# Kernel tuning notes

Measured on AMD Instinct MI355X. Metric: run time of the kernel, lower is better.

## Reference

```python
import jax, jax.numpy as jnp
import numpy as np

HEADS = 12
ROT_DIM = 16  # hidden_dim // num_heads // 4
MAX_FREQ = 256
EPS = 1e-5


def _groupnorm(x, w, b, groups, eps=EPS):
    # x: [B, C, H, W, D]; normalize per (group, H, W, D)
    B, C = x.shape[0], x.shape[1]
    xr = x.reshape(B, groups, -1)
    mu = xr.mean(-1, keepdims=True)
    var = xr.var(-1, keepdims=True)
    xn = ((xr - mu) * jax.lax.rsqrt(var + eps)).reshape(x.shape)
    return xn * w.reshape(1, C, 1, 1, 1) + b.reshape(1, C, 1, 1, 1)


def _layernorm(t, w, b, eps=EPS):
    mu = t.mean(-1, keepdims=True)
    var = t.var(-1, keepdims=True)
    return (t - mu) * jax.lax.rsqrt(var + eps) * w + b


def _rotate_half(t):
    # pairs adjacent elements: (x1, x2) -> (-x2, x1)
    x1 = t[..., 0::2]
    x2 = t[..., 1::2]
    return jnp.stack([-x2, x1], axis=-1).reshape(t.shape)


def _axial_freqs(H, W, D, dim=ROT_DIM, max_freq=MAX_FREQ):
    # 'pixel' rotary: base freqs = linspace(1, max_freq/2, dim//2) * pi, pos in [-1, 1]
    base = jnp.linspace(1.0, max_freq / 2.0, dim // 2) * jnp.pi

    def ax(n):
        pos = jnp.linspace(-1.0, 1.0, n)
        f = pos[:, None] * base[None, :]          # [n, dim//2]
        return jnp.repeat(f, 2, axis=-1)           # [n, dim]

    fh = jnp.broadcast_to(ax(H)[:, None, None, :], (H, W, D, dim))
    fw = jnp.broadcast_to(ax(W)[None, :, None, :], (H, W, D, dim))
    fd = jnp.broadcast_to(ax(D)[None, None, :, :], (H, W, D, dim))
    return jnp.concatenate([fh, fw, fd], -1)       # [H, W, D, 3*dim]


def _rope(freqs, t):
    # t: [B, he, H, W, D, hd]; rotate first rot dims, pass rest through
    rot = freqs.shape[-1]
    tl, tr = t[..., :rot], t[..., rot:]
    tl = tl * jnp.cos(freqs) + _rotate_half(tl) * jnp.sin(freqs)
    return jnp.concatenate([tl, tr], -1)


def setup_inputs() -> dict:
    key = jax.random.key(0)
    ks = jax.random.split(key, 14)
    B, C, H, W, D = 2, 768, 16, 16, 8
    hd = C // HEADS
    f32 = jnp.float32
    inp = {
        "x": jax.random.normal(ks[0], (B, C, H, W, D), f32),
        "norm1_w": 1.0 + 0.1 * jax.random.normal(ks[1], (C,), f32),
        "norm1_b": 0.1 * jax.random.normal(ks[2], (C,), f32),
        "gamma_att": 0.01 * jnp.ones((C,), f32),
        "W_fused": jax.random.normal(ks[3], (C, 7 * C), f32) / np.sqrt(C),
        "b_fused": 0.01 * jax.random.normal(ks[4], (7 * C,), f32),
        "qn_w": 1.0 + 0.1 * jax.random.normal(ks[5], (hd,), f32),
        "qn_b": 0.1 * jax.random.normal(ks[6], (hd,), f32),
        "kn_w": 1.0 + 0.1 * jax.random.normal(ks[7], (hd,), f32),
        "kn_b": 0.1 * jax.random.normal(ks[8], (hd,), f32),
        "W_attn": jax.random.normal(ks[9], (C, C), f32) / np.sqrt(C),
        "W_ffout": jax.random.normal(ks[10], (2 * C, C), f32) / np.sqrt(2 * C),
        "b_ffout": 0.01 * jax.random.normal(ks[11], (C,), f32),
        "bcs": 0,
        "axis_order": 0,
    }
    return inp


def reference(x, norm1_w, norm1_b, gamma_att, W_fused, b_fused, qn_w, qn_b,
              kn_w, kn_b, W_attn, W_ffout, b_ffout, bcs, axis_order):
    B, C, H, W, D = x.shape
    he = HEADS
    hd = C // he
    x_in = x

    # GroupNorm over channels (num_groups = num_heads)
    xn = _groupnorm(x, norm1_w, norm1_b, he)
    t = jnp.transpose(xn, (0, 2, 3, 4, 1))             # b h w d c

    fused = t @ W_fused + b_fused                      # b h w d 7C
    ff, q, k, v = jnp.split(fused, [4 * C, 5 * C, 6 * C], axis=-1)

    def to_heads(z):
        return z.reshape(B, H, W, D, he, hd).transpose(0, 4, 1, 2, 3, 5)  # b he h w d c

    q, k, v = to_heads(q), to_heads(k), to_heads(v)
    q = _layernorm(q, qn_w, qn_b)
    k = _layernorm(k, kn_w, kn_b)

    freqs = _axial_freqs(H, W, D)                      # [H, W, D, 48]
    q = _rope(freqs, q)
    k = _rope(freqs, k)

    S = H * W * D
    qf = q.reshape(B, he, S, hd)
    kf = k.reshape(B, he, S, hd)
    vf = v.reshape(B, he, S, hd)

    scale = 1.0 / np.sqrt(hd)
    scores = jnp.einsum('bhqc,bhkc->bhqk', qf, kf) * scale
    attn = jax.nn.softmax(scores, axis=-1)
    out = jnp.einsum('bhqk,bhkc->bhqc', attn, vf)      # b he S hd

    att = out.reshape(B, he, H, W, D, hd).transpose(0, 2, 3, 4, 1, 5).reshape(B, H, W, D, C)
    att_out = att @ W_attn

    # SwiGLU: first half is value, second half gates
    xh, gate = jnp.split(ff, 2, axis=-1)
    ff_out = (jax.nn.silu(gate) * xh) @ W_ffout + b_ffout

    y = gamma_att * (att_out + ff_out)                 # b h w d c
    return jnp.transpose(y, (0, 4, 1, 2, 3)) + x_in    # b c h w d
```

## Files before the change

kernel.cpp:

```cpp
#include <hip/hip_runtime.h>
#include <hip/hip_bf16.h>

#define HE   12
#define HD   64
#define Cc   768
#define C2   1536
#define C4   3072
#define N7   5376
#define Bb   2
#define Ss   2048
#define BSr  4096
#define PI_F 3.14159265358979f

using f32x4  = __attribute__((ext_vector_type(4))) float;
using short8 = __attribute__((ext_vector_type(8))) short;

__device__ __forceinline__ unsigned short f2b(float f) {
    union { float f; unsigned int u; } v; v.f = f;
    unsigned int u = v.u;
    unsigned int r = (u + 0x7fffu + ((u >> 16) & 1u)) >> 16;
    return (unsigned short)r;
}
__device__ __forceinline__ unsigned short f2bt(float f) {
    union { float f; unsigned int u; } v; v.f = f;
    return (unsigned short)(v.u >> 16);
}
__device__ __forceinline__ float b2f(unsigned short s) {
    union { unsigned int u; float f; } v; v.u = ((unsigned int)s) << 16;
    return v.f;
}
__device__ __forceinline__ f32x4 mfma16(short8 a, short8 b, f32x4 c) {
    return __builtin_amdgcn_mfma_f32_16x16x32_bf16(a, b, c, 0, 0, 0);
}
__device__ __forceinline__ void gl_lds16(const unsigned short* g, unsigned short* l) {
    __builtin_amdgcn_global_load_lds(
        (const __attribute__((address_space(1))) unsigned int*)(const void*)g,
        (__attribute__((address_space(3))) unsigned int*)(void*)l, 16, 0, 0);
}
__device__ __forceinline__ void xcd_tile(int& bx, int& by) {
    int nx = gridDim.x;
    int flat = blockIdx.y * nx + blockIdx.x;
    int nwg = nx * gridDim.y;
    int swz = (flat & 7) * (nwg >> 3) + (flat >> 3);
    bx = swz % nx; by = swz / nx;
}

union U8 { uint4 v; unsigned short u[8]; };

__global__ __launch_bounds__(256) void transpose_w(const float* __restrict__ src,
                                                   unsigned short* __restrict__ dst,
                                                   int R, int Ccol) {
    __shared__ float tile[32][33];
    int tx = threadIdx.x & 31, ty = threadIdx.x >> 5;
    int rt = blockIdx.y * 32, ct = blockIdx.x * 32;
#pragma unroll
    for (int i = 0; i < 4; ++i)
        tile[ty + i * 8][tx] = src[(size_t)(rt + ty + i * 8) * Ccol + ct + tx];
    __syncthreads();
#pragma unroll
    for (int i = 0; i < 4; ++i)
        dst[(size_t)(ct + ty + i * 8) * R + rt + tx] = f2b(tile[tx][ty + i * 8]);
}

__global__ __launch_bounds__(256) void gn_stats(const float* __restrict__ x,
                                                float* __restrict__ stat) {
    int j = blockIdx.x;
    const float4* p = (const float4*)(x + (size_t)j * 131072);
    float s = 0.f, ss = 0.f;
    for (int i = threadIdx.x; i < 32768; i += 256) {
        float4 v = p[i];
        s  += v.x + v.y + v.z + v.w;
        ss += v.x * v.x + v.y * v.y + v.z * v.z + v.w * v.w;
    }
#pragma unroll
    for (int m = 1; m < 64; m <<= 1) { s += __shfl_xor(s, m); ss += __shfl_xor(ss, m); }
    __shared__ float ls[4], lss[4];
    int wid = threadIdx.x >> 6;
    if ((threadIdx.x & 63) == 0) { ls[wid] = s; lss[wid] = ss; }
    __syncthreads();
    if (threadIdx.x == 0) {
        s = ls[0] + ls[1] + ls[2] + ls[3];
        ss = lss[0] + lss[1] + lss[2] + lss[3];
        float mu  = s / 131072.0f;
        float var = ss / 131072.0f - mu * mu;
        stat[j * 2]     = mu;
        stat[j * 2 + 1] = rsqrtf(var + 1e-5f);
    }
}

__global__ __launch_bounds__(256) void norm_transpose(const float* __restrict__ x,
                                                      const float* __restrict__ stat,
                                                      const float* __restrict__ w,
                                                      const float* __restrict__ bgn,
                                                      unsigned short* __restrict__ t) {
    __shared__ float tile[32][33];
    int b = blockIdx.z;
    int st = blockIdx.x * 32, ct = blockIdx.y * 32;
    int tx = threadIdx.x & 31, ty = threadIdx.x >> 5;
#pragma unroll
    for (int i = 0; i < 4; ++i) {
        int c = ct + ty + i * 8;
        int g = c >> 6;
        float mu = stat[(b * 12 + g) * 2], rs = stat[(b * 12 + g) * 2 + 1];
        float v = x[(size_t)(b * Cc + c) * Ss + st + tx];
        tile[ty + i * 8][tx] = (v - mu) * rs * w[c] + bgn[c];
    }
    __syncthreads();
#pragma unroll
    for (int i = 0; i < 4; ++i) {
        int s = st + ty + i * 8, c = ct + tx;
        t[(size_t)(b * Ss + s) * Cc + c] = f2b(tile[tx][ty + i * 8]);
    }
}

template<bool ACCUM, bool BIAS, bool OUTBF16>
__global__ __launch_bounds__(256) void gemm128(const unsigned short* __restrict__ A,
                                               const unsigned short* __restrict__ Bt,
                                               const float* __restrict__ bias,
                                               void* __restrict__ Cout,
                                               int M, int N, int K) {
    __shared__ __align__(16) unsigned short As[128 * 32];
    __shared__ __align__(16) unsigned short Bs[128 * 32];
    const int tid = threadIdx.x;
    const int wid = tid >> 6, lane = tid & 63;
    const int lr = lane & 15, lh = lane >> 4;
    const int wr = wid >> 1, wc = wid & 1;
    int bx, by; xcd_tile(bx, by);
    const int row0 = by * 128, col0 = bx * 128;
    const unsigned short* ga = A  + (size_t)(row0 + (tid >> 2)) * K + (tid & 3) * 8;
    const unsigned short* gb = Bt + (size_t)(col0 + (tid >> 2)) * K + (tid & 3) * 8;
    f32x4 acc[4][4] = {};

    for (int k0 = 0; k0 < K; k0 += 32) {
        gl_lds16(ga + k0,          &As[tid * 8]);
        gl_lds16(ga + 64 * K + k0, &As[2048 + tid * 8]);
        gl_lds16(gb + k0,          &Bs[tid * 8]);
        gl_lds16(gb + 64 * K + k0, &Bs[2048 + tid * 8]);
        __syncthreads();
        short8 af[4], bfr[4];
#pragma unroll
        for (int m = 0; m < 4; ++m) af[m]  = *(const short8*)&As[(wr * 64 + m * 16 + lr) * 32 + lh * 8];
#pragma unroll
        for (int n = 0; n < 4; ++n) bfr[n] = *(const short8*)&Bs[(wc * 64 + n * 16 + lr) * 32 + lh * 8];
#pragma unroll
        for (int m = 0; m < 4; ++m)
#pragma unroll
            for (int n = 0; n < 4; ++n)
                acc[m][n] = mfma16(af[m], bfr[n], acc[m][n]);
        __syncthreads();
    }

#pragma unroll
    for (int m = 0; m < 4; ++m)
#pragma unroll
        for (int n = 0; n < 4; ++n) {
            int row = row0 + wr * 64 + m * 16 + lh * 4;
            int col = col0 + wc * 64 + n * 16 + lr;
            float bv = BIAS ? bias[col] : 0.0f;
#pragma unroll
            for (int r = 0; r < 4; ++r) {
                size_t idx = (size_t)(row + r) * N + col;
                float v = acc[m][n][r] + bv;
                if (ACCUM) v += ((const float*)Cout)[idx];
                if (OUTBF16) ((unsigned short*)Cout)[idx] = f2b(v);
                else         ((float*)Cout)[idx] = v;
            }
        }
}

__global__ __launch_bounds__(256) void gemm_fin(const unsigned short* __restrict__ A,
                                                const unsigned short* __restrict__ Bt,
                                                const float* __restrict__ bo,
                                                const float* __restrict__ oaccIn,
                                                const float* __restrict__ x,
                                                const float* __restrict__ gamma,
                                                float* __restrict__ out,
                                                int M, int N, int K) {
    __shared__ __align__(16) unsigned short As[128 * 32];
    __shared__ __align__(16) unsigned short Bs[128 * 32];
    const int tid = threadIdx.x;
    const int wid = tid >> 6, lane = tid & 63;
    const int lr = lane & 15, lh = lane >> 4;
    const int wr = wid >> 1, wc = wid & 1;
    int bx, by; xcd_tile(bx, by);
    const int row0 = by * 128, col0 = bx * 128;
    const unsigned short* ga = A  + (size_t)(row0 + (tid >> 2)) * K + (tid & 3) * 8;
    const unsigned short* gb = Bt + (size_t)(col0 + (tid >> 2)) * K + (tid & 3) * 8;
    f32x4 acc[4][4] = {};

    for (int k0 = 0; k0 < K; k0 += 32) {
        gl_lds16(ga + k0,          &As[tid * 8]);
        gl_lds16(ga + 64 * K + k0, &As[2048 + tid * 8]);
        gl_lds16(gb + k0,          &Bs[tid * 8]);
        gl_lds16(gb + 64 * K + k0, &Bs[2048 + tid * 8]);
        __syncthreads();
        short8 af[4], bfr[4];
#pragma unroll
        for (int m = 0; m < 4; ++m) af[m]  = *(const short8*)&As[(wr * 64 + m * 16 + lr) * 32 + lh * 8];
#pragma unroll
        for (int n = 0; n < 4; ++n) bfr[n] = *(const short8*)&Bs[(wc * 64 + n * 16 + lr) * 32 + lh * 8];
#pragma unroll
        for (int m = 0; m < 4; ++m)
#pragma unroll
            for (int n = 0; n < 4; ++n)
                acc[m][n] = mfma16(af[m], bfr[n], acc[m][n]);
        __syncthreads();
    }

#pragma unroll
    for (int m = 0; m < 4; ++m)
#pragma unroll
        for (int n = 0; n < 4; ++n) {
            int row = row0 + wr * 64 + m * 16 + lh * 4;
            int col = col0 + wc * 64 + n * 16 + lr;
            float bv = bo[col], gv = gamma[col];
#pragma unroll
            for (int r = 0; r < 4; ++r) {
                int rw = row + r;
                float v = acc[m][n][r] + bv + oaccIn[(size_t)rw * N + col];
                int b = rw >> 11, s = rw & 2047;
                size_t oidx = (size_t)(b * Cc + col) * Ss + s;
                out[oidx] = gv * v + x[oidx];
            }
        }
}

__global__ __launch_bounds__(256) void qkv_prep(const unsigned short* __restrict__ fused,
                                                const float* __restrict__ qnw, const float* __restrict__ qnb,
                                                const float* __restrict__ knw, const float* __restrict__ knb,
                                                unsigned short* __restrict__ qf,
                                                unsigned short* __restrict__ kf,
                                                unsigned short* __restrict__ vf) {
    const int wid = threadIdx.x >> 6, lane = threadIdx.x & 63;
    const int job = blockIdx.x * 4 + wid;
    const int srow = job / 12, h = job % 12;
    const int b = srow >> 11, s = srow & 2047;

    size_t base = (size_t)srow * N7 + C4 + h * HD;
    float qv = b2f(fused[base + lane]);
    float kv = b2f(fused[base + Cc + lane]);
    float vv = b2f(fused[base + 2 * Cc + lane]);

    float qs = qv, ks = kv;
#pragma unroll
    for (int m = 1; m < 64; m <<= 1) { qs += __shfl_xor(qs, m); ks += __shfl_xor(ks, m); }
    float qmu = qs * (1.0f / 64.0f), kmu = ks * (1.0f / 64.0f);
    float qd = qv - qmu, kd = kv - kmu;
    float qv2 = qd * qd, kv2 = kd * kd;
#pragma unroll
    for (int m = 1; m < 64; m <<= 1) { qv2 += __shfl_xor(qv2, m); kv2 += __shfl_xor(kv2, m); }
    float qn = qd * rsqrtf(qv2 * (1.0f / 64.0f) + 1e-5f) * qnw[lane] + qnb[lane];
    float kn = kd * rsqrtf(kv2 * (1.0f / 64.0f) + 1e-5f) * knw[lane] + knb[lane];

    if (lane < 48) {
        int axis = lane >> 4, ii = (lane & 15) >> 1;
        float basef = (1.0f + (float)ii * (127.0f / 7.0f)) * PI_F;
        int   pos_i = (axis == 0) ? (s >> 7) : (axis == 1) ? ((s >> 3) & 15) : (s & 7);
        float denom = (axis == 2) ? 7.0f : 15.0f;
        float pos   = -1.0f + 2.0f * (float)pos_i / denom;
        float ang   = pos * basef;
        float sn, cs;
        sincosf(ang, &sn, &cs);
        float qp = __shfl_xor(qn, 1);
        float kp = __shfl_xor(kn, 1);
        qn = (lane & 1) ? (qn * cs + qp * sn) : (qn * cs - qp * sn);
        kn = (lane & 1) ? (kn * cs + kp * sn) : (kn * cs - kp * sn);
    }

    size_t obase = ((size_t)(b * 12 + h) * Ss + s) * HD + lane;
    qf[obase] = f2b(qn);
    kf[obase] = f2b(kn);
    vf[obase] = f2b(vv);
}

__global__ __launch_bounds__(256) void ffa_prep(const unsigned short* __restrict__ fused,
                                                unsigned short* __restrict__ ffa) {
    int i8 = blockIdx.x * 256 + threadIdx.x;
    int row = i8 / 192, co = (i8 % 192) * 8;
    U8 xa, ga, oa;
    xa.v = *(const uint4*)&fused[(size_t)row * N7 + co];
    ga.v = *(const uint4*)&fused[(size_t)row * N7 + C2 + co];
#pragma unroll
    for (int j = 0; j < 8; ++j) {
        float g = b2f(ga.u[j]);
        float xh = b2f(xa.u[j]);
        float sg = 1.0f / (1.0f + __expf(-g));
        oa.u[j] = f2b(g * sg * xh);
    }
    *(uint4*)&ffa[(size_t)row * C2 + co] = oa.v;
}

__global__ __launch_bounds__(256) void attn64(const unsigned short* __restrict__ qf,
                                              const unsigned short* __restrict__ kf,
                                              const unsigned short* __restrict__ vf,
                                              unsigned short* __restrict__ att) {
    __shared__ __align__(16) unsigned short Ks[2][64][80];
    __shared__ __align__(16) unsigned short Vt[2][64][80];
    __shared__ __align__(16) unsigned short Ps[4][16][80];
    const int tid = threadIdx.x, wid = tid >> 6, lane = tid & 63;
    const int lr = lane & 15, lh = lane >> 4;
    const int bh = blockIdx.y, qt = blockIdx.x;
    const int b = bh / 12, h = bh % 12;
    const size_t kvbase = (size_t)bh * Ss * HD;

    const int qrow = qt * 64 + wid * 16 + lr;
    short8 qa0 = *(const short8*)&qf[kvbase + (size_t)qrow * HD + lh * 8];
    short8 qa1 = *(const short8*)&qf[kvbase + (size_t)qrow * HD + 32 + lh * 8];

    const int r0 = tid >> 3, kc0 = (tid & 7) * 8;
    const int sv0 = (((r0 >> 3) ^ (kc0 >> 3)) << 3) | (r0 & 7);
    const int sv1 = ((((r0 >> 3) + 4) ^ (kc0 >> 3)) << 3) | (r0 & 7);
    const unsigned short* kptr = kf + kvbase + (size_t)r0 * HD + kc0;
    const unsigned short* vptr = vf + kvbase + (size_t)r0 * HD + kc0;

    const short8 ones = {0x3F80, 0x3F80, 0x3F80, 0x3F80, 0x3F80, 0x3F80, 0x3F80, 0x3F80};
    const float c1 = 0.125f * 1.44269504f;
    const float c2 = 23.08312065f;
    const int rxb = (lr >> 2) & 3;

    f32x4 oacc[4] = {};
    f32x4 lacc = {};

    uint4 kreg0 = *(const uint4*)kptr;
    uint4 kreg1 = *(const uint4*)(kptr + 32 * HD);
    U8 vreg0, vreg1;
    vreg0.v = *(const uint4*)vptr;
    vreg1.v = *(const uint4*)(vptr + 32 * HD);
    *(uint4*)&Ks[0][r0][kc0]      = kreg0;
    *(uint4*)&Ks[0][r0 + 32][kc0] = kreg1;
#pragma unroll
    for (int j = 0; j < 8; ++j) Vt[0][kc0 + j][sv0] = vreg0.u[j];
#pragma unroll
    for (int j = 0; j < 8; ++j) Vt[0][kc0 + j][sv1] = vreg1.u[j];
    kreg0   = *(const uint4*)(kptr + 64 * HD);
    kreg1   = *(const uint4*)(kptr + 96 * HD);
    vreg0.v = *(const uint4*)(vptr + 64 * HD);
    vreg1.v = *(const uint4*)(vptr + 96 * HD);
    __syncthreads();

#pragma unroll 2
    for (int kt = 0; kt < 32; ++kt) {
        const int cur = kt & 1;
        if (kt < 31) {
            *(uint4*)&Ks[cur ^ 1][r0][kc0]      = kreg0;
            *(uint4*)&Ks[cur ^ 1][r0 + 32][kc0] = kreg1;
#pragma unroll
            for (int j = 0; j < 8; ++j) Vt[cur ^ 1][kc0 + j][sv0] = vreg0.u[j];
#pragma unroll
            for (int j = 0; j < 8; ++j) Vt[cur ^ 1][kc0 + j][sv1] = vreg1.u[j];
        }
        if (kt < 30) {
            const unsigned short* kp = kptr + (size_t)(kt + 2) * 64 * HD;
            const unsigned short* vp = vptr + (size_t)(kt + 2) * 64 * HD;
            kreg0   = *(const uint4*)kp;
            kreg1   = *(const uint4*)(kp + 32 * HD);
            vreg0.v = *(const uint4*)vp;
            vreg1.v = *(const uint4*)(vp + 32 * HD);
        }

        f32x4 sc[4];
#pragma unroll
        for (int n = 0; n < 4; ++n) {
            f32x4 z = {0.f, 0.f, 0.f, 0.f};
            short8 k0 = *(const short8*)&Ks[cur][n * 16 + lr][lh * 8];
            short8 k1 = *(const short8*)&Ks[cur][n * 16 + lr][32 + lh * 8];
            z = mfma16(qa0, k0, z);
            z = mfma16(qa1, k1, z);
            sc[n] = z;
        }

#pragma unroll
        for (int n = 0; n < 4; ++n)
#pragma unroll
            for (int r = 0; r < 4; ++r)
                sc[n][r] = exp2f(sc[n][r] * c1 - c2);

#pragma unroll
        for (int r = 0; r < 4; ++r) {
            int prow = lh * 4 + r;
            int lo = lr & 7, lr3 = lr >> 3;
            Ps[wid][prow][(((0 + lr3) ^ lh) << 3) | lo] = f2bt(sc[0][r]);
            Ps[wid][prow][(((2 + lr3) ^ lh) << 3) | lo] = f2bt(sc[1][r]);
            Ps[wid][prow][(((4 + lr3) ^ lh) << 3) | lo] = f2bt(sc[2][r]);
            Ps[wid][prow][(((6 + lr3) ^ lh) << 3) | lo] = f2bt(sc[3][r]);
        }

        short8 pa0 = *(const short8*)&Ps[wid][lr][((lh ^ rxb) & 7) * 8];
        short8 pa1 = *(const short8*)&Ps[wid][lr][(((lh + 4) ^ rxb) & 7) * 8];
        lacc = mfma16(pa0, ones, lacc);
        lacc = mfma16(pa1, ones, lacc);
#pragma unroll
        for (int n = 0; n < 4; ++n) {
            int dv = (2 * n + (lr >> 3)) & 7;
            short8 v0 = *(const short8*)&Vt[cur][n * 16 + lr][((lh ^ dv) & 7) * 8];
            short8 v1 = *(const short8*)&Vt[cur][n * 16 + lr][(((lh + 4) ^ dv) & 7) * 8];
            oacc[n] = mfma16(pa0, v0, oacc[n]);
            oacc[n] = mfma16(pa1, v1, oacc[n]);
        }
        __syncthreads();
    }

    float rinv[4];
#pragma unroll
    for (int r = 0; r < 4; ++r) rinv[r] = 1.0f / lacc[r];
#pragma unroll
    for (int n = 0; n < 4; ++n)
#pragma unroll
        for (int r = 0; r < 4; ++r) {
            int srow_w = qt * 64 + wid * 16 + lh * 4 + r;
            int col = h * HD + n * 16 + lr;
            att[(size_t)(b * Ss + srow_w) * Cc + col] = f2b(oacc[n][r] * rinv[r]);
        }
}

extern "C" void kernel_launch(void* const* d_in, const int* in_sizes, int n_in,
                              void* d_out, int out_size, void* d_ws, size_t ws_size,
                              hipStream_t stream) {
    const float* x     = (const float*)d_in[0];
    const float* n1w   = (const float*)d_in[1];
    const float* n1b   = (const float*)d_in[2];
    const float* gamma = (const float*)d_in[3];
    const float* Wf    = (const float*)d_in[4];
    const float* bfu   = (const float*)d_in[5];
    const float* qnw   = (const float*)d_in[6];
    const float* qnb   = (const float*)d_in[7];
    const float* knw   = (const float*)d_in[8];
    const float* knb   = (const float*)d_in[9];
    const float* Wa    = (const float*)d_in[10];
    const float* Wo    = (const float*)d_in[11];
    const float* bo    = (const float*)d_in[12];

    char* ws = (char*)d_ws;
    size_t off = 0;
    auto alloc = [&](size_t bytes) {
        char* p = ws + off;
        off = (off + bytes + 255) & ~(size_t)255;
        return p;
    };
    float*          stat  = (float*)alloc(24 * 2 * 4);
    unsigned short* t     = (unsigned short*)alloc((size_t)BSr * Cc * 2);
    unsigned short* WtF   = (unsigned short*)alloc((size_t)N7 * Cc * 2);
    unsigned short* fused = (unsigned short*)alloc((size_t)BSr * N7 * 2);
    unsigned short* qfB   = (unsigned short*)alloc((size_t)Bb * HE * Ss * HD * 2);
    unsigned short* kfB   = (unsigned short*)alloc((size_t)Bb * HE * Ss * HD * 2);
    unsigned short* vfB   = (unsigned short*)alloc((size_t)Bb * HE * Ss * HD * 2);
    unsigned short* ffa   = (unsigned short*)alloc((size_t)BSr * C2 * 2);
    unsigned short* WtA   = (unsigned short*)alloc((size_t)Cc * Cc * 2);
    unsigned short* WtO   = (unsigned short*)alloc((size_t)Cc * C2 * 2);
    unsigned short* attB  = t;
    float*          oacc  = (float*)fused;

    transpose_w<<<dim3(N7 / 32, Cc / 32), 256, 0, stream>>>(Wf, WtF, Cc, N7);
    transpose_w<<<dim3(Cc / 32, Cc / 32), 256, 0, stream>>>(Wa, WtA, Cc, Cc);
    transpose_w<<<dim3(Cc / 32, C2 / 32), 256, 0, stream>>>(Wo, WtO, C2, Cc);

    gn_stats<<<24, 256, 0, stream>>>(x, stat);
    norm_transpose<<<dim3(Ss / 32, Cc / 32, Bb), 256, 0, stream>>>(x, stat, n1w, n1b, t);

    gemm128<false, true, true><<<dim3(N7 / 128, BSr / 128), 256, 0, stream>>>(
        t, WtF, bfu, fused, BSr, N7, Cc);

    qkv_prep<<<(Bb * Ss * HE) / 4, 256, 0, stream>>>(fused, qnw, qnb, knw, knb, qfB, kfB, vfB);
    ffa_prep<<<(BSr * C2 / 8) / 256, 256, 0, stream>>>(fused, ffa);

    attn64<<<dim3(Ss / 64, Bb * HE), 256, 0, stream>>>(qfB, kfB, vfB, attB);

    gemm128<false, false, false><<<dim3(Cc / 128, BSr / 128), 256, 0, stream>>>(
        attB, WtA, nullptr, oacc, BSr, Cc, Cc);
    gemm_fin<<<dim3(Cc / 128, BSr / 128), 256, 0, stream>>>(
        ffa, WtO, bo, oacc, x, gamma, (float*)d_out, BSr, Cc, C2);
}
```

Measured before the change: 370.8 us.

## Split attention over key halves with combine kernel; double-buffer and swizzle GEMM LDS

Attention is split into two key-range halves via a third grid dimension, each writing unnormalized fp32 partial outputs and row sums to scratch, followed by a combine kernel that sums, normalizes and converts to bf16. This doubles block count to better fill the GPU, at the cost of extra scratch traffic and removal of the attention kernel's LDS double buffering. The GEMM kernels get double-buffered LDS staging with one barrier per step and an XOR swizzle of k-chunks to reduce bank conflicts. Correctness relies on the softmax using a fixed scale without running max, so partials can be summed directly.

```diff
diff --git a/kernel.cpp b/kernel.cpp
--- a/kernel.cpp
+++ b/kernel.cpp
@@ -119,29 +119,40 @@
                                                const float* __restrict__ bias,
                                                void* __restrict__ Cout,
                                                int M, int N, int K) {
-    __shared__ __align__(16) unsigned short As[128 * 32];
-    __shared__ __align__(16) unsigned short Bs[128 * 32];
+    __shared__ __align__(16) unsigned short As[2][128 * 32];
+    __shared__ __align__(16) unsigned short Bs[2][128 * 32];
     const int tid = threadIdx.x;
     const int wid = tid >> 6, lane = tid & 63;
     const int lr = lane & 15, lh = lane >> 4;
     const int wr = wid >> 1, wc = wid & 1;
     int bx, by; xcd_tile(bx, by);
     const int row0 = by * 128, col0 = bx * 128;
-    const unsigned short* ga = A  + (size_t)(row0 + (tid >> 2)) * K + (tid & 3) * 8;
-    const unsigned short* gb = Bt + (size_t)(col0 + (tid >> 2)) * K + (tid & 3) * 8;
+    const int srow = tid >> 2;
+    const int kcs  = (((tid & 3) ^ ((tid >> 3) & 3)) * 8);
+    const unsigned short* ga = A  + (size_t)(row0 + srow) * K + kcs;
+    const unsigned short* gb = Bt + (size_t)(col0 + srow) * K + kcs;
+    const int csw = ((lr >> 1) & 3) << 3;
     f32x4 acc[4][4] = {};
 
+    auto STAGE = [&](int buf, int k0) {
+        gl_lds16(ga + k0,          &As[buf][tid * 8]);
+        gl_lds16(ga + 64 * K + k0, &As[buf][2048 + tid * 8]);
+        gl_lds16(gb + k0,          &Bs[buf][tid * 8]);
+        gl_lds16(gb + 64 * K + k0, &Bs[buf][2048 + tid * 8]);
+    };
+
+    STAGE(0, 0);
+    __syncthreads();
     for (int k0 = 0; k0 < K; k0 += 32) {
-        gl_lds16(ga + k0,          &As[tid * 8]);
-        gl_lds16(ga + 64 * K + k0, &As[2048 + tid * 8]);
-        gl_lds16(gb + k0,          &Bs[tid * 8]);
-        gl_lds16(gb + 64 * K + k0, &Bs[2048 + tid * 8]);
-        __syncthreads();
+        const int cur = (k0 >> 5) & 1;
+        if (k0 + 32 < K) STAGE(cur ^ 1, k0 + 32);
         short8 af[4], bfr[4];
 #pragma unroll
-        for (int m = 0; m < 4; ++m) af[m]  = *(const short8*)&As[(wr * 64 + m * 16 + lr) * 32 + lh * 8];
-#pragma unroll
-        for (int n = 0; n < 4; ++n) bfr[n] = *(const short8*)&Bs[(wc * 64 + n * 16 + lr) * 32 + lh * 8];
+        for (int m = 0; m < 4; ++m)
+            af[m]  = *(const short8*)&As[cur][(wr * 64 + m * 16 + lr) * 32 + ((lh << 3) ^ csw)];
+#pragma unroll
+        for (int n = 0; n < 4; ++n)
+            bfr[n] = *(const short8*)&Bs[cur][(wc * 64 + n * 16 + lr) * 32 + ((lh << 3) ^ csw)];
 #pragma unroll
         for (int m = 0; m < 4; ++m)
 #pragma unroll
@@ -176,29 +187,40 @@
                                                 const float* __restrict__ gamma,
                                                 float* __restrict__ out,
                                                 int M, int N, int K) {
-    __shared__ __align__(16) unsigned short As[128 * 32];
-    __shared__ __align__(16) unsigned short Bs[128 * 32];
+    __shared__ __align__(16) unsigned short As[2][128 * 32];
+    __shared__ __align__(16) unsigned short Bs[2][128 * 32];
     const int tid = threadIdx.x;
     const int wid = tid >> 6, lane = tid & 63;
     const int lr = lane & 15, lh = lane >> 4;
     const int wr = wid >> 1, wc = wid & 1;
     int bx, by; xcd_tile(bx, by);
     const int row0 = by * 128, col0 = bx * 128;
-    const unsigned short* ga = A  + (size_t)(row0 + (tid >> 2)) * K + (tid & 3) * 8;
-    const unsigned short* gb = Bt + (size_t)(col0 + (tid >> 2)) * K + (tid & 3) * 8;
+    const int srow = tid >> 2;
+    const int kcs  = (((tid & 3) ^ ((tid >> 3) & 3)) * 8);
+    const unsigned short* ga = A  + (size_t)(row0 + srow) * K + kcs;
+    const unsigned short* gb = Bt + (size_t)(col0 + srow) * K + kcs;
+    const int csw = ((lr >> 1) & 3) << 3;
     f32x4 acc[4][4] = {};
 
+    auto STAGE = [&](int buf, int k0) {
+        gl_lds16(ga + k0,          &As[buf][tid * 8]);
+        gl_lds16(ga + 64 * K + k0, &As[buf][2048 + tid * 8]);
+        gl_lds16(gb + k0,          &Bs[buf][tid * 8]);
+        gl_lds16(gb + 64 * K + k0, &Bs[buf][2048 + tid * 8]);
+    };
+
+    STAGE(0, 0);
+    __syncthreads();
     for (int k0 = 0; k0 < K; k0 += 32) {
-        gl_lds16(ga + k0,          &As[tid * 8]);
-        gl_lds16(ga + 64 * K + k0, &As[2048 + tid * 8]);
-        gl_lds16(gb + k0,          &Bs[tid * 8]);
-        gl_lds16(gb + 64 * K + k0, &Bs[2048 + tid * 8]);
-        __syncthreads();
+        const int cur = (k0 >> 5) & 1;
+        if (k0 + 32 < K) STAGE(cur ^ 1, k0 + 32);
         short8 af[4], bfr[4];
 #pragma unroll
-        for (int m = 0; m < 4; ++m) af[m]  = *(const short8*)&As[(wr * 64 + m * 16 + lr) * 32 + lh * 8];
-#pragma unroll
-        for (int n = 0; n < 4; ++n) bfr[n] = *(const short8*)&Bs[(wc * 64 + n * 16 + lr) * 32 + lh * 8];
+        for (int m = 0; m < 4; ++m)
+            af[m]  = *(const short8*)&As[cur][(wr * 64 + m * 16 + lr) * 32 + ((lh << 3) ^ csw)];
+#pragma unroll
+        for (int n = 0; n < 4; ++n)
+            bfr[n] = *(const short8*)&Bs[cur][(wc * 64 + n * 16 + lr) * 32 + ((lh << 3) ^ csw)];
 #pragma unroll
         for (int m = 0; m < 4; ++m)
 #pragma unroll
@@ -293,14 +315,13 @@
 __global__ __launch_bounds__(256) void attn64(const unsigned short* __restrict__ qf,
                                               const unsigned short* __restrict__ kf,
                                               const unsigned short* __restrict__ vf,
-                                              unsigned short* __restrict__ att) {
-    __shared__ __align__(16) unsigned short Ks[2][64][80];
-    __shared__ __align__(16) unsigned short Vt[2][64][80];
-    __shared__ __align__(16) unsigned short Ps[4][16][80];
+                                              float* __restrict__ opart) {
+    __shared__ __align__(16) unsigned short Ks[64][72];
+    __shared__ __align__(16) unsigned short Vt[64][72];
+    __shared__ __align__(16) unsigned short Ps[4][16][72];
     const int tid = threadIdx.x, wid = tid >> 6, lane = tid & 63;
     const int lr = lane & 15, lh = lane >> 4;
-    const int bh = blockIdx.y, qt = blockIdx.x;
-    const int b = bh / 12, h = bh % 12;
+    const int bh = blockIdx.y, qt = blockIdx.x, half = blockIdx.z;
     const size_t kvbase = (size_t)bh * Ss * HD;
 
     const int qrow = qt * 64 + wid * 16 + lr;
@@ -310,8 +331,8 @@
     const int r0 = tid >> 3, kc0 = (tid & 7) * 8;
     const int sv0 = (((r0 >> 3) ^ (kc0 >> 3)) << 3) | (r0 & 7);
     const int sv1 = ((((r0 >> 3) + 4) ^ (kc0 >> 3)) << 3) | (r0 & 7);
-    const unsigned short* kptr = kf + kvbase + (size_t)r0 * HD + kc0;
-    const unsigned short* vptr = vf + kvbase + (size_t)r0 * HD + kc0;
+    const unsigned short* kptr = kf + kvbase + (size_t)(half * 16 * 64 + r0) * HD + kc0;
+    const unsigned short* vptr = vf + kvbase + (size_t)(half * 16 * 64 + r0) * HD + kc0;
 
     const short8 ones = {0x3F80, 0x3F80, 0x3F80, 0x3F80, 0x3F80, 0x3F80, 0x3F80, 0x3F80};
     const float c1 = 0.125f * 1.44269504f;
@@ -326,32 +347,19 @@
     U8 vreg0, vreg1;
     vreg0.v = *(const uint4*)vptr;
     vreg1.v = *(const uint4*)(vptr + 32 * HD);
-    *(uint4*)&Ks[0][r0][kc0]      = kreg0;
-    *(uint4*)&Ks[0][r0 + 32][kc0] = kreg1;
-#pragma unroll
-    for (int j = 0; j < 8; ++j) Vt[0][kc0 + j][sv0] = vreg0.u[j];
-#pragma unroll
-    for (int j = 0; j < 8; ++j) Vt[0][kc0 + j][sv1] = vreg1.u[j];
-    kreg0   = *(const uint4*)(kptr + 64 * HD);
-    kreg1   = *(const uint4*)(kptr + 96 * HD);
-    vreg0.v = *(const uint4*)(vptr + 64 * HD);
-    vreg1.v = *(const uint4*)(vptr + 96 * HD);
-    __syncthreads();
-
-#pragma unroll 2
-    for (int kt = 0; kt < 32; ++kt) {
-        const int cur = kt & 1;
-        if (kt < 31) {
-            *(uint4*)&Ks[cur ^ 1][r0][kc0]      = kreg0;
-            *(uint4*)&Ks[cur ^ 1][r0 + 32][kc0] = kreg1;
-#pragma unroll
-            for (int j = 0; j < 8; ++j) Vt[cur ^ 1][kc0 + j][sv0] = vreg0.u[j];
-#pragma unroll
-            for (int j = 0; j < 8; ++j) Vt[cur ^ 1][kc0 + j][sv1] = vreg1.u[j];
-        }
-        if (kt < 30) {
-            const unsigned short* kp = kptr + (size_t)(kt + 2) * 64 * HD;
-            const unsigned short* vp = vptr + (size_t)(kt + 2) * 64 * HD;
+
+    for (int kt = 0; kt < 16; ++kt) {
+        *(uint4*)&Ks[r0][kc0]      = kreg0;
+        *(uint4*)&Ks[r0 + 32][kc0] = kreg1;
+#pragma unroll
+        for (int j = 0; j < 8; ++j) Vt[kc0 + j][sv0] = vreg0.u[j];
+#pragma unroll
+        for (int j = 0; j < 8; ++j) Vt[kc0 + j][sv1] = vreg1.u[j];
+        __syncthreads();
+
+        if (kt < 15) {
+            const unsigned short* kp = kptr + (size_t)(kt + 1) * 64 * HD;
+            const unsigned short* vp = vptr + (size_t)(kt + 1) * 64 * HD;
             kreg0   = *(const uint4*)kp;
             kreg1   = *(const uint4*)(kp + 32 * HD);
             vreg0.v = *(const uint4*)vp;
@@ -362,8 +370,8 @@
 #pragma unroll
         for (int n = 0; n < 4; ++n) {
             f32x4 z = {0.f, 0.f, 0.f, 0.f};
-            short8 k0 = *(const short8*)&Ks[cur][n * 16 + lr][lh * 8];
-            short8 k1 = *(const short8*)&Ks[cur][n * 16 + lr][32 + lh * 8];
+            short8 k0 = *(const short8*)&Ks[n * 16 + lr][lh * 8];
+            short8 k1 = *(const short8*)&Ks[n * 16 + lr][32 + lh * 8];
             z = mfma16(qa0, k0, z);
             z = mfma16(qa1, k1, z);
             sc[n] = z;
@@ -392,25 +400,42 @@
 #pragma unroll
         for (int n = 0; n < 4; ++n) {
             int dv = (2 * n + (lr >> 3)) & 7;
-            short8 v0 = *(const short8*)&Vt[cur][n * 16 + lr][((lh ^ dv) & 7) * 8];
-            short8 v1 = *(const short8*)&Vt[cur][n * 16 + lr][(((lh + 4) ^ dv) & 7) * 8];
+            short8 v0 = *(const short8*)&Vt[n * 16 + lr][((lh ^ dv) & 7) * 8];
+            short8 v1 = *(const short8*)&Vt[n * 16 + lr][(((lh + 4) ^ dv) & 7) * 8];
             oacc[n] = mfma16(pa0, v0, oacc[n]);
             oacc[n] = mfma16(pa1, v1, oacc[n]);
         }
         __syncthreads();
     }
 
-    float rinv[4];
-#pragma unroll
-    for (int r = 0; r < 4; ++r) rinv[r] = 1.0f / lacc[r];
+    const size_t cb = ((size_t)((bh * 32 + qt) * 2 + half)) * 4160;
 #pragma unroll
     for (int n = 0; n < 4; ++n)
 #pragma unroll
-        for (int r = 0; r < 4; ++r) {
-            int srow_w = qt * 64 + wid * 16 + lh * 4 + r;
-            int col = h * HD + n * 16 + lr;
-            att[(size_t)(b * Ss + srow_w) * Cc + col] = f2b(oacc[n][r] * rinv[r]);
-        }
+        for (int r = 0; r < 4; ++r)
+            opart[cb + (size_t)(wid * 16 + lh * 4 + r) * 64 + n * 16 + lr] = oacc[n][r];
+    if (lr == 0)
+#pragma unroll
+        for (int r = 0; r < 4; ++r)
+            opart[cb + 4096 + wid * 16 + lh * 4 + r] = lacc[r];
+}
+
+__global__ __launch_bounds__(256) void att_combine(const float* __restrict__ opart,
+                                                   unsigned short* __restrict__ att) {
+    int i = blockIdx.x * 256 + threadIdx.x;
+    int d4 = i & 15, q = (i >> 4) & 63, qt = (i >> 10) & 31, bh = i >> 15;
+    size_t cb = ((size_t)(bh * 32 + qt) * 2) * 4160;
+    float4 o0 = *(const float4*)&opart[cb + (size_t)q * 64 + d4 * 4];
+    float4 o1 = *(const float4*)&opart[cb + 4160 + (size_t)q * 64 + d4 * 4];
+    float rl = 1.0f / (opart[cb + 4096 + q] + opart[cb + 4160 + 4096 + q]);
+    int b = bh / 12, h = bh % 12;
+    size_t row = (size_t)(b * Ss + qt * 64 + q);
+    ushort4 w;
+    w.x = f2b((o0.x + o1.x) * rl);
+    w.y = f2b((o0.y + o1.y) * rl);
+    w.z = f2b((o0.z + o1.z) * rl);
+    w.w = f2b((o0.w + o1.w) * rl);
+    *(ushort4*)&att[row * Cc + h * HD + d4 * 4] = w;
 }
 
 extern "C" void kernel_launch(void* const* d_in, const int* in_sizes, int n_in,
@@ -449,6 +474,7 @@
     unsigned short* WtO   = (unsigned short*)alloc((size_t)Cc * C2 * 2);
     unsigned short* attB  = t;
     float*          oacc  = (float*)fused;
+    float*          opart = oacc + (size_t)BSr * Cc;
 
     transpose_w<<<dim3(N7 / 32, Cc / 32), 256, 0, stream>>>(Wf, WtF, Cc, N7);
     transpose_w<<<dim3(Cc / 32, Cc / 32), 256, 0, stream>>>(Wa, WtA, Cc, Cc);
@@ -463,7 +489,8 @@
     qkv_prep<<<(Bb * Ss * HE) / 4, 256, 0, stream>>>(fused, qnw, qnb, knw, knb, qfB, kfB, vfB);
     ffa_prep<<<(BSr * C2 / 8) / 256, 256, 0, stream>>>(fused, ffa);
 
-    attn64<<<dim3(Ss / 64, Bb * HE), 256, 0, stream>>>(qfB, kfB, vfB, attB);
+    attn64<<<dim3(Ss / 64, Bb * HE, 2), 256, 0, stream>>>(qfB, kfB, vfB, opart);
+    att_combine<<<3072, 256, 0, stream>>>(opart, attB);
 
     gemm128<false, false, false><<<dim3(Cc / 128, BSr / 128), 256, 0, stream>>>(
         attB, WtA, nullptr, oacc, BSr, Cc, Cc);
```

After: 380.1 us. 2.5% more time.
